# Kernel tuning notes

Measured on AMD Instinct MI355X. Metric: run time of the kernel, lower is better.

Reference implementation:

```python
import jax, jax.numpy as jnp
import numpy as np

OBS_LEN = 8
FUT_LEN = 12
NC = 2            # n_coordinates
S_DIM = 256
Z_DIM = 192
NOISE = 64
H = S_DIM + Z_DIM + NOISE   # 512, pred_lstm_hidden_size
MAP_H = 512                  # hidden_dims[0]
K = 20                       # number of samples (len(pred_lstm_hidden))
N = 2048                     # number of pedestrians
GROUPS = 64


def hard_sigmoid(x):
    return jnp.clip(x / 6.0 + 0.5, 0.0, 1.0)


def hard_tanh(x):
    return jnp.clip(x, -1.0, 1.0)


def setup_inputs() -> dict:
    key = jax.random.key(0)
    ks = jax.random.split(key, 12)
    obs_traj_rel = jax.random.normal(ks[0], (OBS_LEN, N, NC), jnp.float32)
    fut_traj_rel = jax.random.normal(ks[1], (FUT_LEN, N, NC), jnp.float32)
    step = N // GROUPS
    starts = jnp.arange(0, N, step, dtype=jnp.int32)
    seq_start_end = jnp.stack([starts, starts + step], axis=1)  # [GROUPS, 2]
    pred_lstm_hidden = 0.1 * jax.random.normal(ks[2], (K, N, S_DIM + Z_DIM), jnp.float32)
    z_decoder = jax.random.normal(ks[3], (GROUPS, NOISE), jnp.float32)
    # mapping MLP params (init: normal std 0.1, zero bias)
    W1 = 0.1 * jax.random.normal(ks[4], (MAP_H, S_DIM + Z_DIM), jnp.float32)
    b1 = jnp.zeros((MAP_H,), jnp.float32)
    W2 = 0.1 * jax.random.normal(ks[5], (S_DIM + Z_DIM, MAP_H), jnp.float32)
    b2 = jnp.zeros((S_DIM + Z_DIM,), jnp.float32)
    # LSTMCell params
    weight_ih = 0.1 * jax.random.normal(ks[6], (4 * H, NC), jnp.float32)
    weight_hh = 0.1 * jax.random.normal(ks[7], (4 * H, H), jnp.float32)
    bias_ih = jnp.zeros((4 * H,), jnp.float32)
    bias_hh = jnp.zeros((4 * H,), jnp.float32)
    # hidden2pos params
    W_pos = 0.1 * jax.random.normal(ks[8], (NC, H), jnp.float32)
    b_pos = jnp.zeros((NC,), jnp.float32)
    return {
        "obs_traj_rel": obs_traj_rel,
        "fut_traj_rel": fut_traj_rel,
        "seq_start_end": seq_start_end,
        "pred_lstm_hidden": pred_lstm_hidden,
        "z_decoder": z_decoder,
        "W1": W1, "b1": b1, "W2": W2, "b2": b2,
        "weight_ih": weight_ih, "weight_hh": weight_hh,
        "bias_ih": bias_ih, "bias_hh": bias_hh,
        "W_pos": W_pos, "b_pos": b_pos,
    }


def reference(obs_traj_rel, fut_traj_rel, seq_start_end, pred_lstm_hidden,
              z_decoder, W1, b1, W2, b2, weight_ih, weight_hh, bias_ih,
              bias_hh, W_pos, b_pos):
    Kk, Nn, _ = pred_lstm_hidden.shape
    # mapping MLP: Linear -> LeakyReLU -> Linear
    h = jax.nn.leaky_relu(pred_lstm_hidden @ W1.T + b1, negative_slope=0.01)
    h = h @ W2.T + b2                                  # [K, N, S+Z]
    # add_noise: per-group noise vector, concatenated along feature dim
    starts = seq_start_end[:, 0]
    gid = jnp.searchsorted(starts, jnp.arange(Nn), side='right') - 1  # [N]
    noise = jnp.broadcast_to(z_decoder[gid][None], (Kk, Nn, z_decoder.shape[-1]))
    h = jnp.concatenate([h, noise], axis=-1)           # [K, N, H]
    c = jnp.zeros_like(h)
    # initial input: last observed step, repeated over K samples
    inp0 = jnp.broadcast_to(obs_traj_rel[OBS_LEN - 1, :, :NC][None], (Kk, Nn, NC))

    def step(carry, _):
        inp, hh, cc = carry
        gates = inp @ weight_ih.T + bias_ih + hh @ weight_hh.T + bias_hh  # [K,N,4H]
        i, f, g, o = jnp.split(gates, 4, axis=-1)
        cc = hard_sigmoid(f) * cc + hard_sigmoid(i) * hard_tanh(g)
        hh = hard_sigmoid(o) * hard_tanh(cc)
        out = hh @ W_pos.T + b_pos                                        # [K,N,NC]
        return (out, hh, cc), out

    _, outs = jax.lax.scan(step, (inp0, h, c), xs=None, length=FUT_LEN)
    return outs  # [fut_len, K, N, n_coordinates]
```

## Files before the change

kernel.cpp:

```cpp
#include <hip/hip_runtime.h>
#include <stdint.h>

#define OBS_LEN 8
#define FUT_LEN 12
#define DIN     448
#define HDIM    512
#define MAPH    512
#define NAGT    2048
#define MROWS   40960

typedef unsigned short ushort_t;
typedef __attribute__((ext_vector_type(8))) short bf16x8;
typedef __attribute__((ext_vector_type(4))) float f32x4;
typedef __attribute__((ext_vector_type(4))) unsigned short ushort4_t;

__device__ __forceinline__ float hsig(float x)  { return fminf(fmaxf(x * (1.0f/6.0f) + 0.5f, 0.0f), 1.0f); }
__device__ __forceinline__ float htanh(float x) { return fminf(fmaxf(x, -1.0f), 1.0f); }

__device__ __forceinline__ ushort_t f2bf(float f) {
    union { float f; uint32_t u; } v; v.f = f;
    uint32_t r = v.u + 0x7FFFu + ((v.u >> 16) & 1u);
    return (ushort_t)(r >> 16);
}
__device__ __forceinline__ float bf2f(ushort_t u) {
    union { uint32_t u; float f; } v; v.u = ((uint32_t)u) << 16; return v.f;
}
__device__ __forceinline__ ushort4_t cvt4_bf(float4 v) {
    ushort4_t o; o.x = f2bf(v.x); o.y = f2bf(v.y); o.z = f2bf(v.z); o.w = f2bf(v.w);
    return o;
}

#if defined(__has_builtin)
#if __has_builtin(__builtin_amdgcn_global_load_lds)
#define HAVE_GLL 1
#endif
#endif

__device__ __forceinline__ void stage16(const ushort_t* __restrict__ g, ushort_t* l, int lane) {
#ifdef HAVE_GLL
    __builtin_amdgcn_global_load_lds(
        (const __attribute__((address_space(1))) void*)g,
        (__attribute__((address_space(3))) void*)l, 16, 0, 0);
#else
    bf16x8 v = *reinterpret_cast<const bf16x8*>(g);
    *reinterpret_cast<bf16x8*>(l + (size_t)lane * 8) = v;
#endif
}

__global__ void convert_kernel(const float* __restrict__ whh, ushort_t* __restrict__ whh_b,
                               const float* __restrict__ plh, ushort_t* __restrict__ plh_b,
                               const float* __restrict__ W1, ushort_t* __restrict__ W1_b,
                               const float* __restrict__ W2, ushort_t* __restrict__ W2_b,
                               const float* __restrict__ z, ushort_t* __restrict__ h0b)
{
    const long stride = (long)gridDim.x * blockDim.x;
    const long idx = (long)blockIdx.x * blockDim.x + threadIdx.x;

    const long wtot = (long)(4 * HDIM) * HDIM / 4;
    for (long i = idx; i < wtot; i += stride)
        reinterpret_cast<ushort4_t*>(whh_b)[i] = cvt4_bf(reinterpret_cast<const float4*>(whh)[i]);

    const long ptot = (long)MROWS * DIN / 4;
    for (long i = idx; i < ptot; i += stride)
        reinterpret_cast<ushort4_t*>(plh_b)[i] = cvt4_bf(reinterpret_cast<const float4*>(plh)[i]);

    const long w1tot = (long)MAPH * DIN / 4;
    for (long i = idx; i < w1tot; i += stride)
        reinterpret_cast<ushort4_t*>(W1_b)[i] = cvt4_bf(reinterpret_cast<const float4*>(W1)[i]);

    const long w2tot = (long)DIN * MAPH / 4;
    for (long i = idx; i < w2tot; i += stride)
        reinterpret_cast<ushort4_t*>(W2_b)[i] = cvt4_bf(reinterpret_cast<const float4*>(W2)[i]);

    const long ntot = (long)MROWS * 16;
    for (long i = idx; i < ntot; i += stride) {
        long r = i >> 4; int j = (int)(i & 15); int col = DIN + j * 4;
        int n = (int)(r & (NAGT - 1));
        float4 v = *reinterpret_cast<const float4*>(&z[(n >> 5) * 64 + j * 4]);
        *reinterpret_cast<ushort4_t*>(&h0b[r * HDIM + col]) = cvt4_bf(v);
    }
}

template<int ACT>
__global__ __launch_bounds__(256, 2)
void mlp_mfma_kernel(const ushort_t* __restrict__ A, const ushort_t* __restrict__ B,
                     const float* __restrict__ bias, ushort_t* __restrict__ Cb,
                     int Ksz, int ldc)
{
    __shared__ ushort_t sA[128 * 32];
    __shared__ ushort_t sB[64 * 32];

    const int tid  = threadIdx.x;
    const int lane = tid & 63;
    const int wid  = tid >> 6;
    const int wr   = wid >> 1;
    const int wc   = wid & 1;
    const int row0 = blockIdx.x * 128;
    const int col0 = blockIdx.y * 64;

    f32x4 acc[4][2];
#pragma unroll
    for (int mi = 0; mi < 4; ++mi)
#pragma unroll
        for (int ni = 0; ni < 2; ++ni)
            acc[mi][ni] = (f32x4){0.f, 0.f, 0.f, 0.f};

    const int lr4 = lane >> 2;
    const int lk8 = (lane & 3) * 8;

    for (int k0 = 0; k0 < Ksz; k0 += 32) {
        __syncthreads();
#pragma unroll
        for (int cch = 0; cch < 2; ++cch) {
            const int rr = wid * 32 + cch * 16;
            stage16(A + (size_t)(row0 + rr + lr4) * Ksz + k0 + lk8, &sA[rr * 32], lane);
        }
        stage16(B + (size_t)(col0 + wid * 16 + lr4) * Ksz + k0 + lk8, &sB[(wid * 16) * 32], lane);
        __syncthreads();

        bf16x8 ah[4];
#pragma unroll
        for (int mi = 0; mi < 4; ++mi)
            ah[mi] = *reinterpret_cast<const bf16x8*>(
                &sA[(wr * 64 + mi * 16 + (lane & 15)) * 32 + (lane >> 4) * 8]);
#pragma unroll
        for (int ni = 0; ni < 2; ++ni) {
            bf16x8 bfr = *reinterpret_cast<const bf16x8*>(
                &sB[(wc * 32 + ni * 16 + (lane & 15)) * 32 + (lane >> 4) * 8]);
#pragma unroll
            for (int mi = 0; mi < 4; ++mi)
                acc[mi][ni] = __builtin_amdgcn_mfma_f32_16x16x32_bf16(ah[mi], bfr, acc[mi][ni], 0, 0, 0);
        }
    }

#pragma unroll
    for (int mi = 0; mi < 4; ++mi) {
#pragma unroll
        for (int reg = 0; reg < 4; ++reg) {
            int r = row0 + wr * 64 + mi * 16 + (lane >> 4) * 4 + reg;
#pragma unroll
            for (int ni = 0; ni < 2; ++ni) {
                int col = col0 + wc * 32 + ni * 16 + (lane & 15);
                float v = acc[mi][ni][reg] + bias[col];
                if (ACT == 1) v = (v > 0.0f) ? v : 0.01f * v;
                Cb[(size_t)r * ldc + col] = f2bf(v);
            }
        }
    }
}

__global__ __launch_bounds__(256, 2)
void lstm_mfma_kernel(const ushort_t* __restrict__ hin, ushort_t* __restrict__ hout,
                      float* __restrict__ c,
                      const ushort_t* __restrict__ whh_b, const float* __restrict__ wih,
                      const float* __restrict__ bih, const float* __restrict__ bhh,
                      const float* __restrict__ inp, int inp_is_obs)
{
    __shared__ ushort_t sA[128 * 32];
    __shared__ ushort_t sB[4 * 64 * 32];

    const int tid  = threadIdx.x;
    const int lane = tid & 63;
    const int wid  = tid >> 6;
    const int wr   = wid >> 1;
    const int wc   = wid & 1;
    const int row0  = blockIdx.x * 128;
    const int hcol0 = blockIdx.y * 64;

    f32x4 acc[4][4][2];
#pragma unroll
    for (int g = 0; g < 4; ++g)
#pragma unroll
        for (int mi = 0; mi < 4; ++mi)
#pragma unroll
            for (int ni = 0; ni < 2; ++ni)
                acc[g][mi][ni] = (f32x4){0.f, 0.f, 0.f, 0.f};

    const int lr4 = lane >> 2;
    const int lk8 = (lane & 3) * 8;

    for (int k0 = 0; k0 < HDIM; k0 += 32) {
        __syncthreads();
#pragma unroll
        for (int cch = 0; cch < 2; ++cch) {
            const int rr = wid * 32 + cch * 16;
            stage16(hin + (size_t)(row0 + rr + lr4) * HDIM + k0 + lk8, &sA[rr * 32], lane);
        }
#pragma unroll
        for (int cch = 0; cch < 4; ++cch) {
            const int nn = cch * 16;
            stage16(whh_b + ((size_t)wid * HDIM + hcol0 + nn + lr4) * HDIM + k0 + lk8,
                    &sB[(wid * 64 + nn) * 32], lane);
        }
        __syncthreads();

        bf16x8 ah[4];
#pragma unroll
        for (int mi = 0; mi < 4; ++mi) {
            const int ro = (wr * 64 + mi * 16 + (lane & 15)) * 32 + (lane >> 4) * 8;
            ah[mi] = *reinterpret_cast<const bf16x8*>(&sA[ro]);
        }
#pragma unroll
        for (int g = 0; g < 4; ++g) {
#pragma unroll
            for (int ni = 0; ni < 2; ++ni) {
                const int co = (g * 64 + wc * 32 + ni * 16 + (lane & 15)) * 32 + (lane >> 4) * 8;
                bf16x8 bfr = *reinterpret_cast<const bf16x8*>(&sB[co]);
#pragma unroll
                for (int mi = 0; mi < 4; ++mi)
                    acc[g][mi][ni] = __builtin_amdgcn_mfma_f32_16x16x32_bf16(
                        ah[mi], bfr, acc[g][mi][ni], 0, 0, 0);
            }
        }
    }

    float bsum[4][2], wxv[4][2], wyv[4][2];
#pragma unroll
    for (int g = 0; g < 4; ++g)
#pragma unroll
        for (int ni = 0; ni < 2; ++ni) {
            int hc = hcol0 + wc * 32 + ni * 16 + (lane & 15);
            int cg = g * HDIM + hc;
            bsum[g][ni] = bih[cg] + bhh[cg];
            wxv[g][ni] = wih[cg * 2 + 0];
            wyv[g][ni] = wih[cg * 2 + 1];
        }

#pragma unroll
    for (int mi = 0; mi < 4; ++mi) {
#pragma unroll
        for (int reg = 0; reg < 4; ++reg) {
            int r = row0 + wr * 64 + mi * 16 + (lane >> 4) * 4 + reg;
            float ix, iy;
            if (inp_is_obs) {
                int n = r & (NAGT - 1);
                ix = inp[n * 2 + 0]; iy = inp[n * 2 + 1];
            } else {
                ix = inp[(size_t)r * 2 + 0]; iy = inp[(size_t)r * 2 + 1];
            }
#pragma unroll
            for (int ni = 0; ni < 2; ++ni) {
                int hc = hcol0 + wc * 32 + ni * 16 + (lane & 15);
                size_t off = (size_t)r * HDIM + hc;
                float gi = acc[0][mi][ni][reg] + bsum[0][ni] + ix * wxv[0][ni] + iy * wyv[0][ni];
                float gf = acc[1][mi][ni][reg] + bsum[1][ni] + ix * wxv[1][ni] + iy * wyv[1][ni];
                float gg = acc[2][mi][ni][reg] + bsum[2][ni] + ix * wxv[2][ni] + iy * wyv[2][ni];
                float go = acc[3][mi][ni][reg] + bsum[3][ni] + ix * wxv[3][ni] + iy * wyv[3][ni];
                float cc = c[off];
                cc = hsig(gf) * cc + hsig(gi) * htanh(gg);
                float hh = hsig(go) * htanh(cc);
                c[off] = cc;
                hout[off] = f2bf(hh);
            }
        }
    }
}

__global__ __launch_bounds__(256)
void pos_kernel_b(const ushort_t* __restrict__ h, const float* __restrict__ Wp,
                  const float* __restrict__ bp, float* __restrict__ out_t)
{
    int wave = blockIdx.x * 4 + (threadIdx.x >> 6);
    int lane = threadIdx.x & 63;
    bf16x8 hv = *reinterpret_cast<const bf16x8*>(&h[(size_t)wave * HDIM + lane * 8]);
    float hf[8];
#pragma unroll
    for (int j = 0; j < 8; ++j) hf[j] = bf2f((ushort_t)hv[j]);
    float d0 = 0.f, d1 = 0.f;
#pragma unroll
    for (int u = 0; u < 2; ++u) {
        float4 w0 = *reinterpret_cast<const float4*>(&Wp[lane * 8 + u * 4]);
        float4 w1 = *reinterpret_cast<const float4*>(&Wp[HDIM + lane * 8 + u * 4]);
        d0 += hf[u*4+0]*w0.x + hf[u*4+1]*w0.y + hf[u*4+2]*w0.z + hf[u*4+3]*w0.w;
        d1 += hf[u*4+0]*w1.x + hf[u*4+1]*w1.y + hf[u*4+2]*w1.z + hf[u*4+3]*w1.w;
    }
#pragma unroll
    for (int off = 32; off > 0; off >>= 1) {
        d0 += __shfl_xor(d0, off);
        d1 += __shfl_xor(d1, off);
    }
    if (lane == 0) {
        float2 o = make_float2(d0 + bp[0], d1 + bp[1]);
        *reinterpret_cast<float2*>(&out_t[(size_t)wave * 2]) = o;
    }
}

extern "C" void kernel_launch(void* const* d_in, const int* in_sizes, int n_in,
                              void* d_out, int out_size, void* d_ws, size_t ws_size,
                              hipStream_t stream)
{
    const float* obs = (const float*)d_in[0];
    const float* plh = (const float*)d_in[3];
    const float* z   = (const float*)d_in[4];
    const float* W1  = (const float*)d_in[5];
    const float* b1  = (const float*)d_in[6];
    const float* W2  = (const float*)d_in[7];
    const float* b2  = (const float*)d_in[8];
    const float* wih = (const float*)d_in[9];
    const float* whh = (const float*)d_in[10];
    const float* bih = (const float*)d_in[11];
    const float* bhh = (const float*)d_in[12];
    const float* Wp  = (const float*)d_in[13];
    const float* bp  = (const float*)d_in[14];
    float* out = (float*)d_out;

    char* ws = (char*)d_ws;
    const size_t SB_F32  = (size_t)MROWS * HDIM * 4;
    const size_t SB_B16  = (size_t)MROWS * HDIM * 2;
    const size_t SB_WHH  = (size_t)4 * HDIM * HDIM * 2;
    const size_t SB_PLH  = (size_t)MROWS * DIN * 2;
    const size_t SB_W1   = (size_t)MAPH * DIN * 2;
    const size_t SB_W2   = (size_t)DIN * MAPH * 2;
    float*    c_buf = (float*)(ws);
    ushort_t* h0b   = (ushort_t*)(ws + SB_F32);
    ushort_t* h1b   = (ushort_t*)(ws + SB_F32 + SB_B16);
    ushort_t* whh_b = (ushort_t*)(ws + SB_F32 + 2 * SB_B16);
    ushort_t* plh_b = (ushort_t*)(ws + SB_F32 + 2 * SB_B16 + SB_WHH);
    ushort_t* W1_b  = (ushort_t*)(ws + SB_F32 + 2 * SB_B16 + SB_WHH + SB_PLH);
    ushort_t* W2_b  = (ushort_t*)(ws + SB_F32 + 2 * SB_B16 + SB_WHH + SB_PLH + SB_W1);
    ushort_t* Yb    = (ushort_t*)(ws + SB_F32 + 2 * SB_B16 + SB_WHH + SB_PLH + SB_W1 + SB_W2);

    dim3 blk(256);
    convert_kernel<<<2048, 256, 0, stream>>>(whh, whh_b, plh, plh_b, W1, W1_b, W2, W2_b, z, h0b);
    hipMemsetAsync(c_buf, 0, SB_F32, stream);
    mlp_mfma_kernel<1><<<dim3(MROWS / 128, MAPH / 64), blk, 0, stream>>>(
        plh_b, W1_b, b1, Yb, DIN, MAPH);
    mlp_mfma_kernel<0><<<dim3(MROWS / 128, DIN / 64), blk, 0, stream>>>(
        Yb, W2_b, b2, h0b, MAPH, HDIM);

    ushort_t* hin = h0b;
    ushort_t* hout = h1b;
    for (int t = 0; t < FUT_LEN; ++t) {
        const float* inp = (t == 0) ? (obs + (size_t)(OBS_LEN - 1) * NAGT * 2)
                                    : (out + (size_t)(t - 1) * MROWS * 2);
        lstm_mfma_kernel<<<dim3(MROWS / 128, HDIM / 64), blk, 0, stream>>>(
            hin, hout, c_buf, whh_b, wih, bih, bhh, inp, (t == 0) ? 1 : 0);
        pos_kernel_b<<<MROWS / 4, 256, 0, stream>>>(hout, Wp, bp, out + (size_t)t * MROWS * 2);
        ushort_t* tmp = hin; hin = hout; hout = tmp;
    }
}
```

Baseline: 1.784 ms.

## Load LSTM MFMA operands directly from global with register double-buffering

The LSTM recurrent GEMM kernel no longer stages h and W_hh tiles through shared memory with barriers. Each lane now loads its MFMA fragments straight from global memory and prefetches the next k-slice into registers while the current slice is multiplied. The grid is also transposed so that blocks sharing the same rows of h launch next to each other, which should improve L2 reuse of h. In exchange, nothing is shared between waves, so global/L2 traffic and register pressure rise, and the 16-byte per-lane fragment loads are less coalesced.

```diff
diff --git a/kernel.cpp b/kernel.cpp
--- a/kernel.cpp
+++ b/kernel.cpp
@@ -150,22 +150,19 @@
 }
 
 __global__ __launch_bounds__(256, 2)
-void lstm_mfma_kernel(const ushort_t* __restrict__ hin, ushort_t* __restrict__ hout,
-                      float* __restrict__ c,
-                      const ushort_t* __restrict__ whh_b, const float* __restrict__ wih,
-                      const float* __restrict__ bih, const float* __restrict__ bhh,
-                      const float* __restrict__ inp, int inp_is_obs)
-{
-    __shared__ ushort_t sA[128 * 32];
-    __shared__ ushort_t sB[4 * 64 * 32];
-
+void lstm_direct_kernel(const ushort_t* __restrict__ hin, ushort_t* __restrict__ hout,
+                        float* __restrict__ c,
+                        const ushort_t* __restrict__ whh_b, const float* __restrict__ wih,
+                        const float* __restrict__ bih, const float* __restrict__ bhh,
+                        const float* __restrict__ inp, int inp_is_obs)
+{
     const int tid  = threadIdx.x;
     const int lane = tid & 63;
     const int wid  = tid >> 6;
     const int wr   = wid >> 1;
     const int wc   = wid & 1;
-    const int row0  = blockIdx.x * 128;
-    const int hcol0 = blockIdx.y * 64;
+    const int hcol0 = blockIdx.x * 64;
+    const int row0  = blockIdx.y * 128;
 
     f32x4 acc[4][4][2];
 #pragma unroll
@@ -176,43 +173,52 @@
             for (int ni = 0; ni < 2; ++ni)
                 acc[g][mi][ni] = (f32x4){0.f, 0.f, 0.f, 0.f};
 
-    const int lr4 = lane >> 2;
-    const int lk8 = (lane & 3) * 8;
-
-    for (int k0 = 0; k0 < HDIM; k0 += 32) {
-        __syncthreads();
-#pragma unroll
-        for (int cch = 0; cch < 2; ++cch) {
-            const int rr = wid * 32 + cch * 16;
-            stage16(hin + (size_t)(row0 + rr + lr4) * HDIM + k0 + lk8, &sA[rr * 32], lane);
-        }
-#pragma unroll
-        for (int cch = 0; cch < 4; ++cch) {
-            const int nn = cch * 16;
-            stage16(whh_b + ((size_t)wid * HDIM + hcol0 + nn + lr4) * HDIM + k0 + lk8,
-                    &sB[(wid * 64 + nn) * 32], lane);
-        }
-        __syncthreads();
-
-        bf16x8 ah[4];
-#pragma unroll
-        for (int mi = 0; mi < 4; ++mi) {
-            const int ro = (wr * 64 + mi * 16 + (lane & 15)) * 32 + (lane >> 4) * 8;
-            ah[mi] = *reinterpret_cast<const bf16x8*>(&sA[ro]);
-        }
-#pragma unroll
-        for (int g = 0; g < 4; ++g) {
-#pragma unroll
-            for (int ni = 0; ni < 2; ++ni) {
-                const int co = (g * 64 + wc * 32 + ni * 16 + (lane & 15)) * 32 + (lane >> 4) * 8;
-                bf16x8 bfr = *reinterpret_cast<const bf16x8*>(&sB[co]);
+    const ushort_t* Aptr = hin + (size_t)(row0 + wr * 64 + (lane & 15)) * HDIM + ((lane >> 4) * 8);
+    const ushort_t* Bptr = whh_b + (size_t)(hcol0 + wc * 32 + (lane & 15)) * HDIM + ((lane >> 4) * 8);
+
+    bf16x8 a_c[4], b_c[4][2];
+#pragma unroll
+    for (int mi = 0; mi < 4; ++mi)
+        a_c[mi] = *reinterpret_cast<const bf16x8*>(Aptr + (size_t)(mi * 16) * HDIM);
+#pragma unroll
+    for (int g = 0; g < 4; ++g)
+#pragma unroll
+        for (int ni = 0; ni < 2; ++ni)
+            b_c[g][ni] = *reinterpret_cast<const bf16x8*>(Bptr + (size_t)(g * 512 + ni * 16) * HDIM);
+
+    for (int k0 = 0; k0 < HDIM - 32; k0 += 32) {
+        bf16x8 a_n[4], b_n[4][2];
+#pragma unroll
+        for (int mi = 0; mi < 4; ++mi)
+            a_n[mi] = *reinterpret_cast<const bf16x8*>(Aptr + (size_t)(mi * 16) * HDIM + (k0 + 32));
+#pragma unroll
+        for (int g = 0; g < 4; ++g)
+#pragma unroll
+            for (int ni = 0; ni < 2; ++ni)
+                b_n[g][ni] = *reinterpret_cast<const bf16x8*>(Bptr + (size_t)(g * 512 + ni * 16) * HDIM + (k0 + 32));
+#pragma unroll
+        for (int g = 0; g < 4; ++g)
+#pragma unroll
+            for (int ni = 0; ni < 2; ++ni)
 #pragma unroll
                 for (int mi = 0; mi < 4; ++mi)
                     acc[g][mi][ni] = __builtin_amdgcn_mfma_f32_16x16x32_bf16(
-                        ah[mi], bfr, acc[g][mi][ni], 0, 0, 0);
-            }
-        }
-    }
+                        a_c[mi], b_c[g][ni], acc[g][mi][ni], 0, 0, 0);
+#pragma unroll
+        for (int mi = 0; mi < 4; ++mi) a_c[mi] = a_n[mi];
+#pragma unroll
+        for (int g = 0; g < 4; ++g)
+#pragma unroll
+            for (int ni = 0; ni < 2; ++ni) b_c[g][ni] = b_n[g][ni];
+    }
+#pragma unroll
+    for (int g = 0; g < 4; ++g)
+#pragma unroll
+        for (int ni = 0; ni < 2; ++ni)
+#pragma unroll
+            for (int mi = 0; mi < 4; ++mi)
+                acc[g][mi][ni] = __builtin_amdgcn_mfma_f32_16x16x32_bf16(
+                    a_c[mi], b_c[g][ni], acc[g][mi][ni], 0, 0, 0);
 
     float bsum[4][2], wxv[4][2], wyv[4][2];
 #pragma unroll
@@ -333,7 +339,7 @@
     for (int t = 0; t < FUT_LEN; ++t) {
         const float* inp = (t == 0) ? (obs + (size_t)(OBS_LEN - 1) * NAGT * 2)
                                     : (out + (size_t)(t - 1) * MROWS * 2);
-        lstm_mfma_kernel<<<dim3(MROWS / 128, HDIM / 64), blk, 0, stream>>>(
+        lstm_direct_kernel<<<dim3(HDIM / 64, MROWS / 128), blk, 0, stream>>>(
             hin, hout, c_buf, whh_b, wih, bih, bhh, inp, (t == 0) ? 1 : 0);
         pos_kernel_b<<<MROWS / 4, 256, 0, stream>>>(hout, Wp, bp, out + (size_t)t * MROWS * 2);
         ushort_t* tmp = hin; hin = hout; hout = tmp;
```

Result: slower. 3.159 ms (+77.1%).

## Fuse hidden2pos projection into LSTM epilogue and double-buffer LDS tiles

Applied to the files above, without the earlier changes.

Removes the separate per-step position-projection kernel by computing partial dot products of the new hidden state with W_pos in the LSTM epilogue, reducing across 16 lanes and accumulating into the output with atomics (output zeroed beforehand). This avoids re-reading the hidden state and a launch per step. The K-loop also gets double-buffered shared-memory tiles so the next tile is staged while the current one feeds MFMAs, with one barrier per iteration. Costs: extra LDS, atomic contention, and nondeterministic float summation order.

```diff
diff --git a/kernel.cpp b/kernel.cpp
--- a/kernel.cpp
+++ b/kernel.cpp
@@ -150,14 +150,16 @@
 }
 
 __global__ __launch_bounds__(256, 2)
-void lstm_mfma_kernel(const ushort_t* __restrict__ hin, ushort_t* __restrict__ hout,
-                      float* __restrict__ c,
-                      const ushort_t* __restrict__ whh_b, const float* __restrict__ wih,
-                      const float* __restrict__ bih, const float* __restrict__ bhh,
-                      const float* __restrict__ inp, int inp_is_obs)
+void lstm_fused_kernel(const ushort_t* __restrict__ hin, ushort_t* __restrict__ hout,
+                       float* __restrict__ c,
+                       const ushort_t* __restrict__ whh_b, const float* __restrict__ wih,
+                       const float* __restrict__ bih, const float* __restrict__ bhh,
+                       const float* __restrict__ inp, int inp_is_obs,
+                       const float* __restrict__ Wp, const float* __restrict__ bp,
+                       float* __restrict__ out_t)
 {
-    __shared__ ushort_t sA[128 * 32];
-    __shared__ ushort_t sB[4 * 64 * 32];
+    __shared__ ushort_t sA[2][128 * 32];
+    __shared__ ushort_t sB[2][4 * 64 * 32];
 
     const int tid  = threadIdx.x;
     const int lane = tid & 63;
@@ -179,42 +181,49 @@
     const int lr4 = lane >> 2;
     const int lk8 = (lane & 3) * 8;
 
-    for (int k0 = 0; k0 < HDIM; k0 += 32) {
-        __syncthreads();
+    auto STAGE = [&](int b, int k0) {
 #pragma unroll
         for (int cch = 0; cch < 2; ++cch) {
             const int rr = wid * 32 + cch * 16;
-            stage16(hin + (size_t)(row0 + rr + lr4) * HDIM + k0 + lk8, &sA[rr * 32], lane);
+            stage16(hin + (size_t)(row0 + rr + lr4) * HDIM + k0 + lk8, &sA[b][rr * 32], lane);
         }
 #pragma unroll
         for (int cch = 0; cch < 4; ++cch) {
             const int nn = cch * 16;
             stage16(whh_b + ((size_t)wid * HDIM + hcol0 + nn + lr4) * HDIM + k0 + lk8,
-                    &sB[(wid * 64 + nn) * 32], lane);
-        }
-        __syncthreads();
+                    &sB[b][(wid * 64 + nn) * 32], lane);
+        }
+    };
+
+    STAGE(0, 0);
+    __syncthreads();
+
+    for (int kt = 0; kt < 16; ++kt) {
+        const int cur = kt & 1;
+        if (kt < 15) STAGE(cur ^ 1, (kt + 1) * 32);
 
         bf16x8 ah[4];
 #pragma unroll
         for (int mi = 0; mi < 4; ++mi) {
             const int ro = (wr * 64 + mi * 16 + (lane & 15)) * 32 + (lane >> 4) * 8;
-            ah[mi] = *reinterpret_cast<const bf16x8*>(&sA[ro]);
+            ah[mi] = *reinterpret_cast<const bf16x8*>(&sA[cur][ro]);
         }
 #pragma unroll
         for (int g = 0; g < 4; ++g) {
 #pragma unroll
             for (int ni = 0; ni < 2; ++ni) {
                 const int co = (g * 64 + wc * 32 + ni * 16 + (lane & 15)) * 32 + (lane >> 4) * 8;
-                bf16x8 bfr = *reinterpret_cast<const bf16x8*>(&sB[co]);
+                bf16x8 bfr = *reinterpret_cast<const bf16x8*>(&sB[cur][co]);
 #pragma unroll
                 for (int mi = 0; mi < 4; ++mi)
                     acc[g][mi][ni] = __builtin_amdgcn_mfma_f32_16x16x32_bf16(
                         ah[mi], bfr, acc[g][mi][ni], 0, 0, 0);
             }
         }
-    }
-
-    float bsum[4][2], wxv[4][2], wyv[4][2];
+        __syncthreads();
+    }
+
+    float bsum[4][2], wxv[4][2], wyv[4][2], wp0[2], wp1[2];
 #pragma unroll
     for (int g = 0; g < 4; ++g)
 #pragma unroll
@@ -225,6 +234,13 @@
             wxv[g][ni] = wih[cg * 2 + 0];
             wyv[g][ni] = wih[cg * 2 + 1];
         }
+#pragma unroll
+    for (int ni = 0; ni < 2; ++ni) {
+        int hc = hcol0 + wc * 32 + ni * 16 + (lane & 15);
+        wp0[ni] = Wp[hc];
+        wp1[ni] = Wp[HDIM + hc];
+    }
+    const bool addbp = (hcol0 == 0) && (wc == 0);
 
 #pragma unroll
     for (int mi = 0; mi < 4; ++mi) {
@@ -238,6 +254,7 @@
             } else {
                 ix = inp[(size_t)r * 2 + 0]; iy = inp[(size_t)r * 2 + 1];
             }
+            float d0 = 0.f, d1 = 0.f;
 #pragma unroll
             for (int ni = 0; ni < 2; ++ni) {
                 int hc = hcol0 + wc * 32 + ni * 16 + (lane & 15);
@@ -251,37 +268,19 @@
                 float hh = hsig(go) * htanh(cc);
                 c[off] = cc;
                 hout[off] = f2bf(hh);
-            }
-        }
-    }
-}
-
-__global__ __launch_bounds__(256)
-void pos_kernel_b(const ushort_t* __restrict__ h, const float* __restrict__ Wp,
-                  const float* __restrict__ bp, float* __restrict__ out_t)
-{
-    int wave = blockIdx.x * 4 + (threadIdx.x >> 6);
-    int lane = threadIdx.x & 63;
-    bf16x8 hv = *reinterpret_cast<const bf16x8*>(&h[(size_t)wave * HDIM + lane * 8]);
-    float hf[8];
-#pragma unroll
-    for (int j = 0; j < 8; ++j) hf[j] = bf2f((ushort_t)hv[j]);
-    float d0 = 0.f, d1 = 0.f;
-#pragma unroll
-    for (int u = 0; u < 2; ++u) {
-        float4 w0 = *reinterpret_cast<const float4*>(&Wp[lane * 8 + u * 4]);
-        float4 w1 = *reinterpret_cast<const float4*>(&Wp[HDIM + lane * 8 + u * 4]);
-        d0 += hf[u*4+0]*w0.x + hf[u*4+1]*w0.y + hf[u*4+2]*w0.z + hf[u*4+3]*w0.w;
-        d1 += hf[u*4+0]*w1.x + hf[u*4+1]*w1.y + hf[u*4+2]*w1.z + hf[u*4+3]*w1.w;
-    }
-#pragma unroll
-    for (int off = 32; off > 0; off >>= 1) {
-        d0 += __shfl_xor(d0, off);
-        d1 += __shfl_xor(d1, off);
-    }
-    if (lane == 0) {
-        float2 o = make_float2(d0 + bp[0], d1 + bp[1]);
-        *reinterpret_cast<float2*>(&out_t[(size_t)wave * 2]) = o;
+                d0 += hh * wp0[ni];
+                d1 += hh * wp1[ni];
+            }
+#pragma unroll
+            for (int m = 1; m < 16; m <<= 1) {
+                d0 += __shfl_xor(d0, m);
+                d1 += __shfl_xor(d1, m);
+            }
+            if ((lane & 15) == 0) {
+                atomicAdd(&out_t[(size_t)r * 2 + 0], d0 + (addbp ? bp[0] : 0.f));
+                atomicAdd(&out_t[(size_t)r * 2 + 1], d1 + (addbp ? bp[1] : 0.f));
+            }
+        }
     }
 }
 
@@ -323,6 +322,7 @@
     dim3 blk(256);
     convert_kernel<<<2048, 256, 0, stream>>>(whh, whh_b, plh, plh_b, W1, W1_b, W2, W2_b, z, h0b);
     hipMemsetAsync(c_buf, 0, SB_F32, stream);
+    hipMemsetAsync(out, 0, (size_t)out_size * sizeof(float), stream);
     mlp_mfma_kernel<1><<<dim3(MROWS / 128, MAPH / 64), blk, 0, stream>>>(
         plh_b, W1_b, b1, Yb, DIN, MAPH);
     mlp_mfma_kernel<0><<<dim3(MROWS / 128, DIN / 64), blk, 0, stream>>>(
@@ -333,9 +333,9 @@
     for (int t = 0; t < FUT_LEN; ++t) {
         const float* inp = (t == 0) ? (obs + (size_t)(OBS_LEN - 1) * NAGT * 2)
                                     : (out + (size_t)(t - 1) * MROWS * 2);
-        lstm_mfma_kernel<<<dim3(MROWS / 128, HDIM / 64), blk, 0, stream>>>(
-            hin, hout, c_buf, whh_b, wih, bih, bhh, inp, (t == 0) ? 1 : 0);
-        pos_kernel_b<<<MROWS / 4, 256, 0, stream>>>(hout, Wp, bp, out + (size_t)t * MROWS * 2);
+        lstm_fused_kernel<<<dim3(MROWS / 128, HDIM / 64), blk, 0, stream>>>(
+            hin, hout, c_buf, whh_b, wih, bih, bhh, inp, (t == 0) ? 1 : 0,
+            Wp, bp, out + (size_t)t * MROWS * 2);
         ushort_t* tmp = hin; hin = hout; hout = tmp;
     }
 }
```

After: 2.122 ms. 1.19x slower.
